# Kernel tuning notes

Hardware: AMD Instinct MI355X
Metric: run time of the kernel (lower is better)

Reference implementation:

```python
import jax, jax.numpy as jnp
import numpy as np

# Dims: B=4 batch, S=1024 seq, E=512 embed_dim, H=8 heads, K=3 gate lookback.
_B, _S, _E, _H, _K = 4, 1024, 512, 8, 3
_EPS_LN = 1e-5
_DIV_DELTA = 1e-12


def setup_inputs() -> dict:
    key = jax.random.key(0)
    ks = jax.random.split(key, 8)

    def w(k, shape, s=0.02):
        return jax.random.normal(k, shape, jnp.float32) * s

    return {
        "query": jax.random.normal(ks[0], (_B, _S, _E), jnp.float32),
        "ln1_g": jnp.ones((_E,), jnp.float32),
        "ln1_b": jnp.zeros((_E,), jnp.float32),
        "in_proj_w": w(ks[1], (3 * _E, _E)),          # packed W_q;W_k;W_v
        "in_proj_b": jnp.zeros((3 * _E,), jnp.float32),
        "out_w": w(ks[2], (_E, _H * _E)),             # out_proj: Linear(E*H -> E)
        "out_b": jnp.zeros((_E,), jnp.float32),
        "conv_w": w(ks[3], (_H, _E, _K)),             # SyntacticDistanceGate causal conv
        "conv_b": jnp.zeros((_H,), jnp.float32),
        "ln2_g": jnp.ones((_E,), jnp.float32),
        "ln2_b": jnp.zeros((_E,), jnp.float32),
        "mlp_w1": w(ks[4], (4 * _E, _E)),
        "mlp_b1": jnp.zeros((4 * _E,), jnp.float32),
        "mlp_w2": w(ks[5], (_E, 4 * _E)),
        "mlp_b2": jnp.zeros((_E,), jnp.float32),
    }


def _layer_norm(x, g, b):
    m = jnp.mean(x, axis=-1, keepdims=True)
    v = jnp.mean(jnp.square(x - m), axis=-1, keepdims=True)
    return (x - m) * jax.lax.rsqrt(v + _EPS_LN) * g + b


def _syntactic_gate(x, conv_w, conv_b):
    """x: [B,S,E] -> gate [B,H,S,S], distance [B,H,S].
    Causal depth-to-head conv produces per-head syntactic distances; gate is a
    smooth comparison sigmoid(d_i - d_j) (PRPN-style distance gating)."""
    K = conv_w.shape[-1]
    xp = jnp.pad(x, ((0, 0), (K - 1, 0), (0, 0)))  # causal left pad
    S = x.shape[1]
    d = conv_b[None, :, None]
    for k in range(K):  # tiny fixed lookback loop
        d = d + jnp.einsum("bse,he->bhs", xp[:, k:k + S, :], conv_w[:, :, k])
    distance = jnp.tanh(d)                               # [B,H,S]
    gate = jax.nn.sigmoid(distance[:, :, :, None] - distance[:, :, None, :])
    return gate, distance


def reference(query, ln1_g, ln1_b, in_proj_w, in_proj_b, out_w, out_b,
              conv_w, conv_b, ln2_g, ln2_b, mlp_w1, mlp_b1, mlp_w2, mlp_b2):
    B, S, E = query.shape
    H = conv_w.shape[0]

    nq = _layer_norm(query, ln1_g, ln1_b)  # self-attention: key=value=normed query

    gate, _distance = _syntactic_gate(nq, conv_w, conv_b)  # [B,H,S,S]

    # In-projections (heads are NOT split: each head sees full E-dim q/k/v).
    qkv = nq @ in_proj_w.T + in_proj_b          # [B,S,3E]
    q, k, v = jnp.split(qkv, 3, axis=-1)

    # Raw scores (scaled by sqrt(E), per source). Identical across heads since
    # q/k are merely repeated per head; compute once and broadcast over H.
    scores = jnp.einsum("bie,bje->bij", q, k) / jnp.sqrt(jnp.float32(E))

    # NOTE: with no key_padding_mask the source skips softmax entirely; the
    # gate multiplies RAW scores, then sum-normalizes.
    w = scores[:, None, :, :] * gate                       # [B,H,S,S]
    w = w / (jnp.sum(w, axis=-1, keepdims=True) + _DIV_DELTA)

    ctx = jnp.einsum("bhij,bje->bhie", w, v)               # [B,H,S,E]
    # torch: chunk over head-major dim 0 then cat on features -> [B,S,H*E]
    ctx = jnp.transpose(ctx, (0, 2, 1, 3)).reshape(B, S, H * E)
    attn_out = ctx @ out_w.T + out_b                       # [B,S,E]

    x = query + attn_out                                   # layer_scale_1 = Identity
    h = _layer_norm(x, ln2_g, ln2_b)
    h = jax.nn.gelu(h @ mlp_w1.T + mlp_b1, approximate=False)
    x = x + (h @ mlp_w2.T + mlp_b2)                        # layer_scale_2 = Identity
    return x
```

## Files before the change

### kernel.cpp

```cpp
#include <hip/hip_runtime.h>
#include <math.h>

#define SQ 1024
#define EE 512
#define NB 4
#define NH 8

typedef __attribute__((ext_vector_type(8))) short bfrag;
typedef __attribute__((ext_vector_type(4))) float f32x4;
typedef __attribute__((ext_vector_type(4))) unsigned short u16x4;
typedef __attribute__((ext_vector_type(8))) unsigned short u16x8;

typedef __attribute__((address_space(3))) unsigned int lds_u32;
typedef const __attribute__((address_space(1))) unsigned int glb_u32;

__device__ __forceinline__ float sep(float x) {
  asm volatile("" : "+v"(x));
  return x;
}

__device__ __forceinline__ unsigned short f2bf(float f) {
  unsigned u = __builtin_bit_cast(unsigned, f);
  unsigned r = (u + 0x7fffu + ((u >> 16) & 1u)) >> 16;
  return (unsigned short)r;
}
__device__ __forceinline__ float bf2f(unsigned short h) {
  unsigned u = ((unsigned)h) << 16;
  return __builtin_bit_cast(float, u);
}
__device__ __forceinline__ float bitf(unsigned u) { return __builtin_bit_cast(float, u); }

__device__ __forceinline__ unsigned cvtpk(float a, float b) {
  unsigned r;
  asm("v_cvt_pk_bf16_f32 %0, %1, %2" : "=v"(r) : "v"(a), "v"(b));
  return r;
}

__device__ __forceinline__ void split4(float4 v, u16x4& h, u16x4& l) {
  h.x = f2bf(v.x); l.x = f2bf(v.x - bf2f(h.x));
  h.y = f2bf(v.y); l.y = f2bf(v.y - bf2f(h.y));
  h.z = f2bf(v.z); l.z = f2bf(v.z - bf2f(h.z));
  h.w = f2bf(v.w); l.w = f2bf(v.w - bf2f(h.w));
}

__device__ __forceinline__ int swzi(int row, int c8) {
  return row * 40 + ((c8 ^ ((row >> 2) & 6)) << 2);
}

__global__ __launch_bounds__(64) void ln_np(const float* __restrict__ x,
                                            const float* __restrict__ g,
                                            const float* __restrict__ b,
                                            float* __restrict__ y) {
  __shared__ float xs[EE];
  __shared__ float bc[2];
  long long t = blockIdx.x;
  int lane = threadIdx.x;
#pragma unroll
  for (int m = 0; m < 8; m++) xs[lane + 64 * m] = x[t * EE + lane + 64 * m];
  __syncthreads();
  int l = lane >> 3, a = lane & 7;
  float r = 0.f;
  if (lane < 32) {
    r = xs[l * 128 + a];
#pragma unroll
    for (int m = 1; m < 16; m++) r = r + xs[l * 128 + 8 * m + a];
  }
  r = r + __shfl_xor(r, 1);
  r = r + __shfl_xor(r, 2);
  r = r + __shfl_xor(r, 4);
  r = r + __shfl_xor(r, 8);
  r = r + __shfl_xor(r, 16);
  if (lane == 0) bc[0] = r / 512.0f;
  __syncthreads();
  float mean = bc[0];
  r = 0.f;
  if (lane < 32) {
#pragma unroll
    for (int m = 0; m < 16; m++) {
      float d = sep(xs[l * 128 + 8 * m + a] - mean);
      float s2 = sep(d * d);
      r = (m == 0) ? s2 : (r + s2);
    }
  }
  r = r + __shfl_xor(r, 1);
  r = r + __shfl_xor(r, 2);
  r = r + __shfl_xor(r, 4);
  r = r + __shfl_xor(r, 8);
  r = r + __shfl_xor(r, 16);
  if (lane == 0) bc[1] = r / 512.0f;
  __syncthreads();
  float var = bc[1];
  float rs = 1.0f / sqrtf(var + 1e-5f);
#pragma unroll
  for (int m = 0; m < 8; m++) {
    int i = lane + 64 * m;
    float d = sep(xs[i] - mean);
    float t1 = sep(d * rs);
    float t2 = sep(t1 * g[i]);
    y[t * EE + i] = t2 + b[i];
  }
}

__global__ __launch_bounds__(64) void ln_np_s(const float* __restrict__ x,
                                              const float* __restrict__ g,
                                              const float* __restrict__ b,
                                              unsigned short* __restrict__ yh,
                                              unsigned short* __restrict__ yl) {
  __shared__ float xs[EE];
  __shared__ float bc[2];
  long long t = blockIdx.x;
  int lane = threadIdx.x;
#pragma unroll
  for (int m = 0; m < 8; m++) xs[lane + 64 * m] = x[t * EE + lane + 64 * m];
  __syncthreads();
  int l = lane >> 3, a = lane & 7;
  float r = 0.f;
  if (lane < 32) {
    r = xs[l * 128 + a];
#pragma unroll
    for (int m = 1; m < 16; m++) r = r + xs[l * 128 + 8 * m + a];
  }
  r = r + __shfl_xor(r, 1);
  r = r + __shfl_xor(r, 2);
  r = r + __shfl_xor(r, 4);
  r = r + __shfl_xor(r, 8);
  r = r + __shfl_xor(r, 16);
  if (lane == 0) bc[0] = r / 512.0f;
  __syncthreads();
  float mean = bc[0];
  r = 0.f;
  if (lane < 32) {
#pragma unroll
    for (int m = 0; m < 16; m++) {
      float d = sep(xs[l * 128 + 8 * m + a] - mean);
      float s2 = sep(d * d);
      r = (m == 0) ? s2 : (r + s2);
    }
  }
  r = r + __shfl_xor(r, 1);
  r = r + __shfl_xor(r, 2);
  r = r + __shfl_xor(r, 4);
  r = r + __shfl_xor(r, 8);
  r = r + __shfl_xor(r, 16);
  if (lane == 0) bc[1] = r / 512.0f;
  __syncthreads();
  float var = bc[1];
  float rs = 1.0f / sqrtf(var + 1e-5f);
#pragma unroll
  for (int m = 0; m < 8; m++) {
    int i = lane + 64 * m;
    float d = sep(xs[i] - mean);
    float t1 = sep(d * rs);
    float t2 = sep(t1 * g[i]);
    float o = t2 + b[i];
    unsigned short hh = f2bf(o);
    yh[t * EE + i] = hh;
    yl[t * EE + i] = f2bf(o - bf2f(hh));
  }
}

__global__ __launch_bounds__(256) void dist_np(const float* __restrict__ nq,
                                               const float* __restrict__ conv_w,
                                               const float* __restrict__ conv_b,
                                               float* __restrict__ dist,
                                               float* __restrict__ Edist) {
  int bh = blockIdx.x;
  int b = bh >> 3, h = bh & 7;
  float cb = conv_b[h];
  const float* W = conv_w + (long long)h * EE * 3;
  int s = blockIdx.y * 256 + threadIdx.x;
  float d = cb;
#pragma unroll
  for (int k = 0; k < 3; k++) {
    int t = s - 2 + k;
    if (t < 0) continue;
    const float* row = nq + ((long long)b * SQ + t) * EE;
    float acc = 0.f;
    for (int e = 0; e < EE; e++) acc = __builtin_fmaf(row[e], W[e * 3 + k], acc);
    d = sep(d + acc);
  }
  float dv = (float)tanh((double)d);
  dist[(long long)bh * SQ + s] = dv;
  Edist[(long long)bh * SQ + s] = __expf(dv);
}

__device__ __forceinline__ float gelu_exact(float x) {
  return 0.5f * x * (1.f + erff(x / 1.41421356237309504880f));
}

template <int ACT, int SPLITK>
__global__ __launch_bounds__(256) void gemm_nt(const float* __restrict__ A, int lda, long long sA,
                                               const float* __restrict__ B, int ldb, long long sB,
                                               const float* __restrict__ bias,
                                               const float* __restrict__ Res,
                                               float* __restrict__ C, int ldc, long long sC,
                                               int K, float alpha) {
  __shared__ float As[16][68];
  __shared__ float Bs[16][68];
  int z = blockIdx.z;
  A += (long long)z * sA;
  B += (long long)z * sB;
  C += (long long)z * sC;
  int m0 = blockIdx.y * 64, n0 = blockIdx.x * 64;
  int tid = threadIdx.x;
  int lr = tid >> 2, lc = tid & 3;
  int tx = tid & 15, ty = tid >> 4;
  float acc[4][4] = {};
  float acc2[4][4] = {};
  const float* Arow = A + (long long)(m0 + lr) * lda + lc * 4;
  const float* Brow = B + (long long)(n0 + lr) * ldb + lc * 4;
  float4 a4 = *(const float4*)(Arow);
  float4 b4 = *(const float4*)(Brow);
  for (int k0 = 0; k0 < K; k0 += 16) {
    __syncthreads();
    As[lc * 4 + 0][lr] = a4.x; As[lc * 4 + 1][lr] = a4.y;
    As[lc * 4 + 2][lr] = a4.z; As[lc * 4 + 3][lr] = a4.w;
    Bs[lc * 4 + 0][lr] = b4.x; Bs[lc * 4 + 1][lr] = b4.y;
    Bs[lc * 4 + 2][lr] = b4.z; Bs[lc * 4 + 3][lr] = b4.w;
    __syncthreads();
    int kn = (k0 + 16 < K) ? (k0 + 16) : k0;
    float4 a4n = *(const float4*)(Arow + kn);
    float4 b4n = *(const float4*)(Brow + kn);
    float(*tgt)[4] = (SPLITK > 0 && k0 >= SPLITK) ? acc2 : acc;
#pragma unroll
    for (int kk = 0; kk < 16; kk++) {
      float4 av = *(const float4*)&As[kk][ty * 4];
      float4 bv = *(const float4*)&Bs[kk][tx * 4];
      float a[4] = {av.x, av.y, av.z, av.w};
      float bb[4] = {bv.x, bv.y, bv.z, bv.w};
#pragma unroll
      for (int i = 0; i < 4; i++)
#pragma unroll
        for (int j = 0; j < 4; j++) tgt[i][j] += a[i] * bb[j];
    }
    a4 = a4n;
    b4 = b4n;
  }
  if (SPLITK > 0) {
#pragma unroll
    for (int i = 0; i < 4; i++)
#pragma unroll
      for (int j = 0; j < 4; j++) acc[i][j] = sep(acc[i][j]) + acc2[i][j];
  }
  float4 bias4 = make_float4(0.f, 0.f, 0.f, 0.f);
  if (ACT != 2 && bias) bias4 = *(const float4*)(bias + n0 + tx * 4);
#pragma unroll
  for (int i = 0; i < 4; i++) {
    int row = m0 + ty * 4 + i;
    float o[4];
    if (ACT == 2) {
#pragma unroll
      for (int j = 0; j < 4; j++) o[j] = acc[i][j] / alpha;
    } else {
      o[0] = sep(acc[i][0] * alpha) + bias4.x;
      o[1] = sep(acc[i][1] * alpha) + bias4.y;
      o[2] = sep(acc[i][2] * alpha) + bias4.z;
      o[3] = sep(acc[i][3] * alpha) + bias4.w;
    }
    if (ACT == 1) {
#pragma unroll
      for (int j = 0; j < 4; j++) o[j] = gelu_exact(o[j]);
    }
    if (Res) {
      float4 r4 = *(const float4*)(Res + (long long)row * ldc + n0 + tx * 4);
      o[0] = sep(o[0]) + r4.x; o[1] = sep(o[1]) + r4.y;
      o[2] = sep(o[2]) + r4.z; o[3] = sep(o[3]) + r4.w;
    }
    *(float4*)(C + (long long)row * ldc + n0 + tx * 4) = make_float4(o[0], o[1], o[2], o[3]);
  }
}

__global__ __launch_bounds__(64) void rowsum_np(const float* __restrict__ scores,
                                                const float* __restrict__ dist,
                                                float* __restrict__ invrs) {
  __shared__ float wsm[SQ];
  int i = blockIdx.x;
  int z = blockIdx.y;
  int b = z >> 3;
  const float* srow = scores + ((long long)b * SQ + i) * SQ;
  const float* dz = dist + (long long)z * SQ;
  float di = dz[i];
  int lane = threadIdx.x;
#pragma unroll
  for (int m = 0; m < 16; m++) {
    int j = lane + 64 * m;
    float e = (float)exp((double)(dz[j] - di));
    float gg = 1.f / (1.f + e);
    wsm[j] = srow[j] * gg;
  }
  __syncthreads();
  int l = lane >> 3, a = lane & 7;
  float r = wsm[l * 128 + a];
#pragma unroll
  for (int m = 1; m < 16; m++) r = r + wsm[l * 128 + 8 * m + a];
  r = r + __shfl_xor(r, 1);
  r = r + __shfl_xor(r, 2);
  r = r + __shfl_xor(r, 4);
  r = r + __shfl_xor(r, 8);
  r = r + __shfl_xor(r, 16);
  r = r + __shfl_xor(r, 32);
  if (lane == 0) invrs[(long long)z * SQ + i] = 1.f / (r + 1e-12f);
}

__global__ __launch_bounds__(256) void vsplit_t(const float* __restrict__ qkv,
                                                unsigned short* __restrict__ VhT,
                                                unsigned short* __restrict__ VlT) {
  __shared__ float tile[64][65];
  int b = blockIdx.z;
  int j0 = blockIdx.x * 64;
  int e0 = blockIdx.y * 64;
  const float* V = qkv + (long long)b * SQ * (3 * EE) + 2 * EE;
  unsigned short* Vh = VhT + (long long)b * EE * SQ;
  unsigned short* Vl = VlT + (long long)b * EE * SQ;
  int tx = threadIdx.x & 15, ty = threadIdx.x >> 4;
#pragma unroll
  for (int r = 0; r < 4; r++) {
    int j = j0 + ty + r * 16;
    float4 v = *(const float4*)(V + (long long)j * (3 * EE) + e0 + tx * 4);
    tile[ty + r * 16][tx * 4 + 0] = v.x;
    tile[ty + r * 16][tx * 4 + 1] = v.y;
    tile[ty + r * 16][tx * 4 + 2] = v.z;
    tile[ty + r * 16][tx * 4 + 3] = v.w;
  }
  __syncthreads();
#pragma unroll
  for (int r = 0; r < 4; r++) {
    int el = ty + r * 16;
    float4 f;
    f.x = tile[tx * 4 + 0][el];
    f.y = tile[tx * 4 + 1][el];
    f.z = tile[tx * 4 + 2][el];
    f.w = tile[tx * 4 + 3][el];
    u16x4 hh, ll;
    split4(f, hh, ll);
    long long o = (long long)(e0 + el) * SQ + j0 + tx * 4;
    *(u16x4*)(Vh + o) = hh;
    *(u16x4*)(Vl + o) = ll;
  }
}

__global__ __launch_bounds__(256) void wsplit(const float* __restrict__ W,
                                              unsigned short* __restrict__ Wh,
                                              unsigned short* __restrict__ Wl, int n4) {
  int i = blockIdx.x * 256 + threadIdx.x;
  if (i >= n4) return;
  float4 v = *(const float4*)(W + (long long)i * 4);
  u16x4 h, l;
  split4(v, h, l);
  *(u16x4*)(Wh + (long long)i * 4) = h;
  *(u16x4*)(Wl + (long long)i * 4) = l;
}

__global__ __launch_bounds__(256, 2) void ctx_bf3(const float* __restrict__ scores,
                                                  const float* __restrict__ Edist,
                                                  const float* __restrict__ invrs,
                                                  const unsigned short* __restrict__ VhT,
                                                  const unsigned short* __restrict__ VlT,
                                                  unsigned short* __restrict__ Ch,
                                                  unsigned short* __restrict__ Cl) {
  __shared__ __align__(16) unsigned short Ah[128 * 40], Al[128 * 40];
  __shared__ __align__(16) unsigned short Bh[256 * 40], Bl[256 * 40];
  int z = blockIdx.z, b = z >> 3, h = z & 7;
  const float* Sb = scores + (long long)b * SQ * SQ;
  const unsigned short* Vh = VhT + (long long)b * EE * SQ;
  const unsigned short* Vl = VlT + (long long)b * EE * SQ;
  unsigned short* Chb = Ch + (long long)b * SQ * (NH * EE) + h * EE;
  unsigned short* Clb = Cl + (long long)b * SQ * (NH * EE) + h * EE;
  const float* Ez = Edist + (long long)z * SQ;
  int m0 = blockIdx.y * 128, n0 = blockIdx.x * 256;
  int tid = threadIdx.x;
  int wave = tid >> 6, lane = tid & 63;
  int quad = lane >> 4, l16 = lane & 15;
  f32x4 acc[4][8];
#pragma unroll
  for (int mf = 0; mf < 4; mf++)
#pragma unroll
    for (int nf = 0; nf < 8; nf++) acc[mf][nf] = (f32x4)(0.f);

  int aam = tid & 127, aakc = tid >> 7;
  float ei = Ez[m0 + aam];
  float inv = invrs[(long long)z * SQ + m0 + aam];
  float ci = ei * inv;
  const float* Srow = Sb + (long long)(m0 + aam) * SQ;
  int brow = tid;
  const unsigned short* VhRow = Vh + (long long)(n0 + brow) * SQ;
  const unsigned short* VlRow = Vl + (long long)(n0 + brow) * SQ;

  uint2 aHp[4], aLp[4];
  u16x8 bH[4], bL[4];

  auto loadconv = [&](int kb) {
#pragma unroll
    for (int r = 0; r < 4; r++) {
      int kc = aakc * 4 + r;
      float4 s4 = *(const float4*)(Srow + kb + kc * 4);
      float4 e4 = *(const float4*)(Ez + kb + kc * 4);
      float ax = (s4.x * ci) * __builtin_amdgcn_rcpf(ei + e4.x);
      float ay = (s4.y * ci) * __builtin_amdgcn_rcpf(ei + e4.y);
      float az = (s4.z * ci) * __builtin_amdgcn_rcpf(ei + e4.z);
      float aw = (s4.w * ci) * __builtin_amdgcn_rcpf(ei + e4.w);
      unsigned h01 = cvtpk(ax, ay), h23 = cvtpk(az, aw);
      float hx = bitf(h01 << 16), hy = bitf(h01 & 0xffff0000u);
      float hz = bitf(h23 << 16), hw = bitf(h23 & 0xffff0000u);
      unsigned l01 = cvtpk(ax - hx, ay - hy), l23 = cvtpk(az - hz, aw - hw);
      aHp[r] = make_uint2(h01, h23);
      aLp[r] = make_uint2(l01, l23);
    }
#pragma unroll
    for (int c = 0; c < 4; c++) {
      bH[c] = *(const u16x8*)(VhRow + kb + c * 8);
      bL[c] = *(const u16x8*)(VlRow + kb + c * 8);
    }
  };

  loadconv(0);
  for (int k0 = 0; k0 < SQ; k0 += 32) {
    __syncthreads();
#pragma unroll
    for (int r = 0; r < 4; r++) {
      *(uint2*)&Ah[swzi(aam, aakc * 4 + r)] = aHp[r];
      *(uint2*)&Al[swzi(aam, aakc * 4 + r)] = aLp[r];
    }
#pragma unroll
    for (int c = 0; c < 4; c++) {
      *(u16x8*)&Bh[swzi(brow, 2 * c)] = bH[c];
      *(u16x8*)&Bl[swzi(brow, 2 * c)] = bL[c];
    }
    __syncthreads();
    int kn = (k0 + 32 < SQ) ? (k0 + 32) : k0;
    loadconv(kn);
    bfrag ah[4], al_[4];
#pragma unroll
    for (int mf = 0; mf < 4; mf++) {
      int ra = (wave >> 1) * 64 + mf * 16 + l16;
      ah[mf] = *(const bfrag*)&Ah[swzi(ra, quad * 2)];
      al_[mf] = *(const bfrag*)&Al[swzi(ra, quad * 2)];
    }
#pragma unroll
    for (int nf = 0; nf < 8; nf++) {
      int rb = (wave & 1) * 128 + nf * 16 + l16;
      bfrag bh = *(const bfrag*)&Bh[swzi(rb, quad * 2)];
      bfrag bl = *(const bfrag*)&Bl[swzi(rb, quad * 2)];
#pragma unroll
      for (int mf = 0; mf < 4; mf++) {
        acc[mf][nf] = __builtin_amdgcn_mfma_f32_16x16x32_bf16(al_[mf], bh, acc[mf][nf], 0, 0, 0);
        acc[mf][nf] = __builtin_amdgcn_mfma_f32_16x16x32_bf16(ah[mf], bl, acc[mf][nf], 0, 0, 0);
        acc[mf][nf] = __builtin_amdgcn_mfma_f32_16x16x32_bf16(ah[mf], bh, acc[mf][nf], 0, 0, 0);
      }
    }
  }
#pragma unroll
  for (int mf = 0; mf < 4; mf++) {
#pragma unroll
    for (int nf = 0; nf < 8; nf++) {
      int col = n0 + (wave & 1) * 128 + nf * 16 + l16;
#pragma unroll
      for (int r = 0; r < 4; r++) {
        int row = m0 + (wave >> 1) * 64 + mf * 16 + quad * 4 + r;
        float o = acc[mf][nf][r];
        unsigned short hh = f2bf(o);
        Chb[(long long)row * (NH * EE) + col] = hh;
        Clb[(long long)row * (NH * EE) + col] = f2bf(o - bf2f(hh));
      }
    }
  }
}

template <int ACT, int OUTM>
__global__ __launch_bounds__(256) void gemm_bf3w(
    const unsigned short* __restrict__ Ah_g, const unsigned short* __restrict__ Al_g, int lda,
    const unsigned short* __restrict__ Bh_g, const unsigned short* __restrict__ Bl_g, int ldb,
    const float* __restrict__ bias, const float* __restrict__ Res,
    float* __restrict__ C, unsigned short* __restrict__ Ch, unsigned short* __restrict__ Cl,
    int ldc, int K) {
  __shared__ __align__(16) unsigned short lds[3 * 12288];
  int gx = gridDim.x;
  int nwg = gx * (int)gridDim.y;
  int lin = blockIdx.y * gx + blockIdx.x;
  int cpx = nwg >> 3;
  int tl = (lin & 7) * cpx + (lin >> 3);
  int bx = tl % gx, by = tl / gx;
  int m0 = by * 128, n0 = bx * 64;
  int tid = threadIdx.x, wave = tid >> 6, lane = tid & 63;
  int quad = lane >> 4, l16 = lane & 15;

  const unsigned short* gptr[6];
  int ldsoff[6];
#pragma unroll
  for (int i = 0; i < 6; i++) {
    int d = wave * 6 + i;
    const unsigned short* src;
    int rowbase, ld, tb, qt;
    if (d < 8)       { src = Ah_g; rowbase = m0; ld = lda; tb = 0;     qt = d; }
    else if (d < 16) { src = Al_g; rowbase = m0; ld = lda; tb = 4096;  qt = d - 8; }
    else if (d < 20) { src = Bh_g; rowbase = n0; ld = ldb; tb = 8192;  qt = d - 16; }
    else             { src = Bl_g; rowbase = n0; ld = ldb; tb = 10240; qt = d - 20; }
    int row = qt * 16 + (lane >> 2);
    int cG = (lane & 3) ^ ((row >> 1) & 3);
    gptr[i] = src + (long long)(rowbase + row) * ld + cG * 8;
    ldsoff[i] = tb + qt * 512;
  }

  auto stage = [&](int buf, int kb) {
#pragma unroll
    for (int i = 0; i < 6; i++)
      __builtin_amdgcn_global_load_lds((glb_u32*)(gptr[i] + kb),
                                       (lds_u32*)&lds[buf * 12288 + ldsoff[i]], 16, 0, 0);
  };

  int aoff[4], boff[2];
#pragma unroll
  for (int mf = 0; mf < 4; mf++) {
    int r = (wave >> 1) * 64 + mf * 16 + l16;
    aoff[mf] = r * 32 + ((quad ^ ((r >> 1) & 3)) * 8);
  }
#pragma unroll
  for (int nf = 0; nf < 2; nf++) {
    int r = (wave & 1) * 32 + nf * 16 + l16;
    boff[nf] = r * 32 + ((quad ^ ((r >> 1) & 3)) * 8);
  }

  f32x4 acc[4][2];
#pragma unroll
  for (int mf = 0; mf < 4; mf++)
#pragma unroll
    for (int nf = 0; nf < 2; nf++) acc[mf][nf] = (f32x4)(0.f);

  int NT = K >> 5;
  stage(0, 0);
  stage(1, 32);
  int cur = 0;
  for (int t = 0; t < NT; t++) {
    int nb = cur + 2; if (nb >= 3) nb -= 3;
    int kf = (t + 2 < NT) ? (t + 2) * 32 : (NT - 1) * 32;
    stage(nb, kf);
    asm volatile("s_waitcnt vmcnt(12)" ::: "memory");
    __builtin_amdgcn_s_barrier();
    __builtin_amdgcn_sched_barrier(0);
    const unsigned short* L = &lds[cur * 12288];
    bfrag bh[2], bl[2];
#pragma unroll
    for (int nf = 0; nf < 2; nf++) {
      bh[nf] = *(const bfrag*)&L[8192 + boff[nf]];
      bl[nf] = *(const bfrag*)&L[10240 + boff[nf]];
    }
#pragma unroll
    for (int mf = 0; mf < 4; mf++) {
      bfrag ah = *(const bfrag*)&L[aoff[mf]];
      bfrag al = *(const bfrag*)&L[4096 + aoff[mf]];
#pragma unroll
      for (int nf = 0; nf < 2; nf++) {
        acc[mf][nf] = __builtin_amdgcn_mfma_f32_16x16x32_bf16(al, bh[nf], acc[mf][nf], 0, 0, 0);
        acc[mf][nf] = __builtin_amdgcn_mfma_f32_16x16x32_bf16(ah, bl[nf], acc[mf][nf], 0, 0, 0);
        acc[mf][nf] = __builtin_amdgcn_mfma_f32_16x16x32_bf16(ah, bh[nf], acc[mf][nf], 0, 0, 0);
      }
    }
    __builtin_amdgcn_sched_barrier(0);
    __builtin_amdgcn_s_barrier();
    cur++; if (cur >= 3) cur -= 3;
  }

#pragma unroll
  for (int mf = 0; mf < 4; mf++) {
#pragma unroll
    for (int nf = 0; nf < 2; nf++) {
      int col = n0 + (wave & 1) * 32 + nf * 16 + l16;
      float bi = bias ? bias[col] : 0.f;
#pragma unroll
      for (int r = 0; r < 4; r++) {
        int row = m0 + (wave >> 1) * 64 + mf * 16 + quad * 4 + r;
        float o = acc[mf][nf][r] + bi;
        if (ACT == 1) o = gelu_exact(o);
        if (OUTM == 0) {
          if (Res) o = o + Res[(long long)row * ldc + col];
          C[(long long)row * ldc + col] = o;
        } else {
          unsigned short hh = f2bf(o);
          Ch[(long long)row * ldc + col] = hh;
          Cl[(long long)row * ldc + col] = f2bf(o - bf2f(hh));
        }
      }
    }
  }
}

extern "C" void kernel_launch(void* const* d_in, const int* in_sizes, int n_in,
                              void* d_out, int out_size, void* d_ws, size_t ws_size,
                              hipStream_t stream) {
  const float* query     = (const float*)d_in[0];
  const float* ln1_g     = (const float*)d_in[1];
  const float* ln1_b     = (const float*)d_in[2];
  const float* in_proj_w = (const float*)d_in[3];
  const float* in_proj_b = (const float*)d_in[4];
  const float* out_w     = (const float*)d_in[5];
  const float* out_b     = (const float*)d_in[6];
  const float* conv_w    = (const float*)d_in[7];
  const float* conv_b    = (const float*)d_in[8];
  const float* ln2_g     = (const float*)d_in[9];
  const float* ln2_b     = (const float*)d_in[10];
  const float* mlp_w1    = (const float*)d_in[11];
  const float* mlp_b1    = (const float*)d_in[12];
  const float* mlp_w2    = (const float*)d_in[13];
  const float* mlp_b2    = (const float*)d_in[14];
  float* out = (float*)d_out;
  char* ws = (char*)d_ws;

  float* nq     = (float*)(ws + 0);
  float* qkv    = (float*)(ws + (8ull << 20));
  float* dist   = (float*)(ws + (32ull << 20));
  float* invrs  = (float*)(ws + (32ull << 20) + 131072);
  float* scores = (float*)(ws + (32ull << 20) + 262144);
  unsigned short* VhT = (unsigned short*)(ws + 0);
  unsigned short* VlT = (unsigned short*)(ws + (4ull << 20));
  unsigned short* ctxh = (unsigned short*)(ws + (48ull << 20) + 262144);
  unsigned short* ctxl = (unsigned short*)(ws + (80ull << 20) + 262144);
  unsigned short* out_wh = (unsigned short*)(ws + (32ull << 20) + 262144);
  unsigned short* out_wl = out_wh + 2097152;
  unsigned short* w1h    = out_wl + 2097152;
  unsigned short* w1l    = w1h + 1048576;
  unsigned short* w2h    = w1l + 1048576;
  unsigned short* w2l    = w2h + 1048576;
  unsigned short* ln2h = (unsigned short*)(ws + (48ull << 20) + 262144);
  unsigned short* ln2l = ln2h + 2097152;
  unsigned short* hbufh = (unsigned short*)(ws + 0);
  unsigned short* hbufl = hbufh + 8388608;
  float* Edist = (float*)d_out;

  ln_np<<<dim3(NB * SQ), 64, 0, stream>>>(query, ln1_g, ln1_b, nq);
  dist_np<<<dim3(NB * NH, 4), 256, 0, stream>>>(nq, conv_w, conv_b, dist, Edist);
  gemm_nt<0, 384><<<dim3(24, 64, 1), 256, 0, stream>>>(nq, EE, 0, in_proj_w, EE, 0,
                                                       in_proj_b, nullptr, qkv, 3 * EE, 0, EE, 1.f);
  vsplit_t<<<dim3(16, 8, NB), 256, 0, stream>>>(qkv, VhT, VlT);
  gemm_nt<2, 384><<<dim3(16, 16, NB), 256, 0, stream>>>(
      qkv, 3 * EE, (long long)SQ * 3 * EE, qkv + EE, 3 * EE, (long long)SQ * 3 * EE,
      nullptr, nullptr, scores, SQ, (long long)SQ * SQ, EE, sqrtf(512.0f));
  rowsum_np<<<dim3(SQ, NB * NH), 64, 0, stream>>>(scores, dist, invrs);
  ctx_bf3<<<dim3(2, 8, NB * NH), 256, 0, stream>>>(scores, Edist, invrs, VhT, VlT, ctxh, ctxl);
  wsplit<<<dim3(2048), 256, 0, stream>>>(out_w, out_wh, out_wl, 524288);
  wsplit<<<dim3(1024), 256, 0, stream>>>(mlp_w1, w1h, w1l, 262144);
  wsplit<<<dim3(1024), 256, 0, stream>>>(mlp_w2, w2h, w2l, 262144);
  gemm_bf3w<0, 0><<<dim3(8, 32), 256, 0, stream>>>(ctxh, ctxl, NH * EE, out_wh, out_wl, NH * EE,
                                                   out_b, query, out, nullptr, nullptr,
                                                   EE, NH * EE);
  ln_np_s<<<dim3(NB * SQ), 64, 0, stream>>>(out, ln2_g, ln2_b, ln2h, ln2l);
  gemm_bf3w<1, 1><<<dim3(32, 32), 256, 0, stream>>>(ln2h, ln2l, EE, w1h, w1l, EE,
                                                    mlp_b1, nullptr, nullptr, hbufh, hbufl,
                                                    4 * EE, EE);
  gemm_bf3w<0, 0><<<dim3(8, 32), 256, 0, stream>>>(hbufh, hbufl, 4 * EE, w2h, w2l, 4 * EE,
                                                   mlp_b2, out, out, nullptr, nullptr,
                                                   EE, 4 * EE);
}
```

Before: 669.4 us.

## Split-K two-group GEMM for long-K projections and 512-thread ctx kernel

Adds gemm_bf3w2, which runs two 256-thread groups per block, each covering half of K with its own triple-buffered LDS pipeline. The two partial sums are reduced through LDS before the epilogue. It is used for the out_proj and MLP-down GEMMs, which have a long K and only 256 blocks each. Separately, ctx_bf3 moves to 512 threads with 8 waves on a 2x4 wave grid, smaller per-wave tiles, an unpadded XOR-swizzled LDS layout and precomputed offsets. The goal is more waves in flight to hide latency, at the cost of doubled LDS use per block and an extra reduction step.

```diff
diff --git a/kernel.cpp b/kernel.cpp
--- a/kernel.cpp
+++ b/kernel.cpp
@@ -41,10 +41,6 @@
   h.y = f2bf(v.y); l.y = f2bf(v.y - bf2f(h.y));
   h.z = f2bf(v.z); l.z = f2bf(v.z - bf2f(h.z));
   h.w = f2bf(v.w); l.w = f2bf(v.w - bf2f(h.w));
-}
-
-__device__ __forceinline__ int swzi(int row, int c8) {
-  return row * 40 + ((c8 ^ ((row >> 2) & 6)) << 2);
 }
 
 __global__ __launch_bounds__(64) void ln_np(const float* __restrict__ x,
@@ -351,15 +347,15 @@
   *(u16x4*)(Wl + (long long)i * 4) = l;
 }
 
-__global__ __launch_bounds__(256, 2) void ctx_bf3(const float* __restrict__ scores,
-                                                  const float* __restrict__ Edist,
-                                                  const float* __restrict__ invrs,
-                                                  const unsigned short* __restrict__ VhT,
-                                                  const unsigned short* __restrict__ VlT,
-                                                  unsigned short* __restrict__ Ch,
-                                                  unsigned short* __restrict__ Cl) {
-  __shared__ __align__(16) unsigned short Ah[128 * 40], Al[128 * 40];
-  __shared__ __align__(16) unsigned short Bh[256 * 40], Bl[256 * 40];
+__global__ __launch_bounds__(512) void ctx_bf3(const float* __restrict__ scores,
+                                               const float* __restrict__ Edist,
+                                               const float* __restrict__ invrs,
+                                               const unsigned short* __restrict__ VhT,
+                                               const unsigned short* __restrict__ VlT,
+                                               unsigned short* __restrict__ Ch,
+                                               unsigned short* __restrict__ Cl) {
+  __shared__ __align__(16) unsigned short Ah[128 * 32], Al[128 * 32];
+  __shared__ __align__(16) unsigned short Bh[256 * 32], Bl[256 * 32];
   int z = blockIdx.z, b = z >> 3, h = z & 7;
   const float* Sb = scores + (long long)b * SQ * SQ;
   const unsigned short* Vh = VhT + (long long)b * EE * SQ;
@@ -371,28 +367,29 @@
   int tid = threadIdx.x;
   int wave = tid >> 6, lane = tid & 63;
   int quad = lane >> 4, l16 = lane & 15;
-  f32x4 acc[4][8];
+  int wr = wave >> 2, wc = wave & 3;
+  f32x4 acc[4][4];
 #pragma unroll
   for (int mf = 0; mf < 4; mf++)
 #pragma unroll
-    for (int nf = 0; nf < 8; nf++) acc[mf][nf] = (f32x4)(0.f);
+    for (int nf = 0; nf < 4; nf++) acc[mf][nf] = (f32x4)(0.f);
 
   int aam = tid & 127, aakc = tid >> 7;
   float ei = Ez[m0 + aam];
   float inv = invrs[(long long)z * SQ + m0 + aam];
   float ci = ei * inv;
   const float* Srow = Sb + (long long)(m0 + aam) * SQ;
-  int brow = tid;
+  int brow = tid & 255, bk8 = tid >> 8;
   const unsigned short* VhRow = Vh + (long long)(n0 + brow) * SQ;
   const unsigned short* VlRow = Vl + (long long)(n0 + brow) * SQ;
 
-  uint2 aHp[4], aLp[4];
-  u16x8 bH[4], bL[4];
+  uint2 aHp[2], aLp[2];
+  u16x8 bH[2], bL[2];
 
   auto loadconv = [&](int kb) {
 #pragma unroll
-    for (int r = 0; r < 4; r++) {
-      int kc = aakc * 4 + r;
+    for (int r = 0; r < 2; r++) {
+      int kc = aakc * 2 + r;
       float4 s4 = *(const float4*)(Srow + kb + kc * 4);
       float4 e4 = *(const float4*)(Ez + kb + kc * 4);
       float ax = (s4.x * ci) * __builtin_amdgcn_rcpf(ei + e4.x);
@@ -407,24 +404,44 @@
       aLp[r] = make_uint2(l01, l23);
     }
 #pragma unroll
-    for (int c = 0; c < 4; c++) {
-      bH[c] = *(const u16x8*)(VhRow + kb + c * 8);
-      bL[c] = *(const u16x8*)(VlRow + kb + c * 8);
+    for (int r = 0; r < 2; r++) {
+      bH[r] = *(const u16x8*)(VhRow + kb + (bk8 * 2 + r) * 8);
+      bL[r] = *(const u16x8*)(VlRow + kb + (bk8 * 2 + r) * 8);
     }
   };
+
+  int offA = aam * 32 + ((aakc ^ ((aam >> 1) & 3)) * 8);
+  int offB[2];
+#pragma unroll
+  for (int r = 0; r < 2; r++) {
+    int c = bk8 * 2 + r;
+    offB[r] = brow * 32 + ((c ^ ((brow >> 1) & 3)) * 8);
+  }
+  int aoff[4], boff[4];
+#pragma unroll
+  for (int mf = 0; mf < 4; mf++) {
+    int ra = wr * 64 + mf * 16 + l16;
+    aoff[mf] = ra * 32 + ((quad ^ ((ra >> 1) & 3)) * 8);
+  }
+#pragma unroll
+  for (int nf = 0; nf < 4; nf++) {
+    int rb = wc * 64 + nf * 16 + l16;
+    boff[nf] = rb * 32 + ((quad ^ ((rb >> 1) & 3)) * 8);
+  }
 
   loadconv(0);
   for (int k0 = 0; k0 < SQ; k0 += 32) {
     __syncthreads();
-#pragma unroll
-    for (int r = 0; r < 4; r++) {
-      *(uint2*)&Ah[swzi(aam, aakc * 4 + r)] = aHp[r];
-      *(uint2*)&Al[swzi(aam, aakc * 4 + r)] = aLp[r];
-    }
-#pragma unroll
-    for (int c = 0; c < 4; c++) {
-      *(u16x8*)&Bh[swzi(brow, 2 * c)] = bH[c];
-      *(u16x8*)&Bl[swzi(brow, 2 * c)] = bL[c];
+    {
+      uint4 hv = make_uint4(aHp[0].x, aHp[0].y, aHp[1].x, aHp[1].y);
+      uint4 lv = make_uint4(aLp[0].x, aLp[0].y, aLp[1].x, aLp[1].y);
+      *(uint4*)&Ah[offA] = hv;
+      *(uint4*)&Al[offA] = lv;
+    }
+#pragma unroll
+    for (int r = 0; r < 2; r++) {
+      *(u16x8*)&Bh[offB[r]] = bH[r];
+      *(u16x8*)&Bl[offB[r]] = bL[r];
     }
     __syncthreads();
     int kn = (k0 + 32 < SQ) ? (k0 + 32) : k0;
@@ -432,15 +449,13 @@
     bfrag ah[4], al_[4];
 #pragma unroll
     for (int mf = 0; mf < 4; mf++) {
-      int ra = (wave >> 1) * 64 + mf * 16 + l16;
-      ah[mf] = *(const bfrag*)&Ah[swzi(ra, quad * 2)];
-      al_[mf] = *(const bfrag*)&Al[swzi(ra, quad * 2)];
-    }
-#pragma unroll
-    for (int nf = 0; nf < 8; nf++) {
-      int rb = (wave & 1) * 128 + nf * 16 + l16;
-      bfrag bh = *(const bfrag*)&Bh[swzi(rb, quad * 2)];
-      bfrag bl = *(const bfrag*)&Bl[swzi(rb, quad * 2)];
+      ah[mf] = *(const bfrag*)&Ah[aoff[mf]];
+      al_[mf] = *(const bfrag*)&Al[aoff[mf]];
+    }
+#pragma unroll
+    for (int nf = 0; nf < 4; nf++) {
+      bfrag bh = *(const bfrag*)&Bh[boff[nf]];
+      bfrag bl = *(const bfrag*)&Bl[boff[nf]];
 #pragma unroll
       for (int mf = 0; mf < 4; mf++) {
         acc[mf][nf] = __builtin_amdgcn_mfma_f32_16x16x32_bf16(al_[mf], bh, acc[mf][nf], 0, 0, 0);
@@ -452,11 +467,11 @@
 #pragma unroll
   for (int mf = 0; mf < 4; mf++) {
 #pragma unroll
-    for (int nf = 0; nf < 8; nf++) {
-      int col = n0 + (wave & 1) * 128 + nf * 16 + l16;
+    for (int nf = 0; nf < 4; nf++) {
+      int col = n0 + wc * 64 + nf * 16 + l16;
 #pragma unroll
       for (int r = 0; r < 4; r++) {
-        int row = m0 + (wave >> 1) * 64 + mf * 16 + quad * 4 + r;
+        int row = m0 + wr * 64 + mf * 16 + quad * 4 + r;
         float o = acc[mf][nf][r];
         unsigned short hh = f2bf(o);
         Chb[(long long)row * (NH * EE) + col] = hh;
@@ -578,6 +593,149 @@
           unsigned short hh = f2bf(o);
           Ch[(long long)row * ldc + col] = hh;
           Cl[(long long)row * ldc + col] = f2bf(o - bf2f(hh));
+        }
+      }
+    }
+  }
+}
+
+template <int ACT, int OUTM>
+__global__ __launch_bounds__(512) void gemm_bf3w2(
+    const unsigned short* __restrict__ Ah_g, const unsigned short* __restrict__ Al_g, int lda,
+    const unsigned short* __restrict__ Bh_g, const unsigned short* __restrict__ Bl_g, int ldb,
+    const float* __restrict__ bias, const float* __restrict__ Res,
+    float* __restrict__ C, unsigned short* __restrict__ Ch, unsigned short* __restrict__ Cl,
+    int ldc, int K) {
+  __shared__ __align__(16) unsigned short lds[2][3 * 12288];
+  int gx = gridDim.x;
+  int nwg = gx * (int)gridDim.y;
+  int lin = blockIdx.y * gx + blockIdx.x;
+  int cpx = nwg >> 3;
+  int tl = (lin & 7) * cpx + (lin >> 3);
+  int bx = tl % gx, by = tl / gx;
+  int m0 = by * 128, n0 = bx * 64;
+  int tid = threadIdx.x;
+  int grp = tid >> 8, gtid = tid & 255;
+  int wave = gtid >> 6, lane = tid & 63;
+  int quad = lane >> 4, l16 = lane & 15;
+  int kbase = grp * (K >> 1);
+
+  const unsigned short* gptr[6];
+  int ldsoff[6];
+#pragma unroll
+  for (int i = 0; i < 6; i++) {
+    int d = wave * 6 + i;
+    const unsigned short* src;
+    int rowbase, ld, tb, qt;
+    if (d < 8)       { src = Ah_g; rowbase = m0; ld = lda; tb = 0;     qt = d; }
+    else if (d < 16) { src = Al_g; rowbase = m0; ld = lda; tb = 4096;  qt = d - 8; }
+    else if (d < 20) { src = Bh_g; rowbase = n0; ld = ldb; tb = 8192;  qt = d - 16; }
+    else             { src = Bl_g; rowbase = n0; ld = ldb; tb = 10240; qt = d - 20; }
+    int row = qt * 16 + (lane >> 2);
+    int cG = (lane & 3) ^ ((row >> 1) & 3);
+    gptr[i] = src + (long long)(rowbase + row) * ld + cG * 8;
+    ldsoff[i] = tb + qt * 512;
+  }
+
+  auto stage = [&](int buf, int kb) {
+#pragma unroll
+    for (int i = 0; i < 6; i++)
+      __builtin_amdgcn_global_load_lds((glb_u32*)(gptr[i] + kb),
+                                       (lds_u32*)&lds[grp][buf * 12288 + ldsoff[i]], 16, 0, 0);
+  };
+
+  int aoff[4], boff[2];
+#pragma unroll
+  for (int mf = 0; mf < 4; mf++) {
+    int r = (wave >> 1) * 64 + mf * 16 + l16;
+    aoff[mf] = r * 32 + ((quad ^ ((r >> 1) & 3)) * 8);
+  }
+#pragma unroll
+  for (int nf = 0; nf < 2; nf++) {
+    int r = (wave & 1) * 32 + nf * 16 + l16;
+    boff[nf] = r * 32 + ((quad ^ ((r >> 1) & 3)) * 8);
+  }
+
+  f32x4 acc[4][2];
+#pragma unroll
+  for (int mf = 0; mf < 4; mf++)
+#pragma unroll
+    for (int nf = 0; nf < 2; nf++) acc[mf][nf] = (f32x4)(0.f);
+
+  int NT = (K >> 1) >> 5;
+  stage(0, kbase);
+  stage(1, kbase + 32);
+  int cur = 0;
+  for (int t = 0; t < NT; t++) {
+    int nb = cur + 2; if (nb >= 3) nb -= 3;
+    int kf = (t + 2 < NT) ? (t + 2) * 32 : (NT - 1) * 32;
+    stage(nb, kbase + kf);
+    asm volatile("s_waitcnt vmcnt(12)" ::: "memory");
+    __builtin_amdgcn_s_barrier();
+    __builtin_amdgcn_sched_barrier(0);
+    const unsigned short* L = &lds[grp][cur * 12288];
+    bfrag bh[2], bl[2];
+#pragma unroll
+    for (int nf = 0; nf < 2; nf++) {
+      bh[nf] = *(const bfrag*)&L[8192 + boff[nf]];
+      bl[nf] = *(const bfrag*)&L[10240 + boff[nf]];
+    }
+#pragma unroll
+    for (int mf = 0; mf < 4; mf++) {
+      bfrag ah = *(const bfrag*)&L[aoff[mf]];
+      bfrag al = *(const bfrag*)&L[4096 + aoff[mf]];
+#pragma unroll
+      for (int nf = 0; nf < 2; nf++) {
+        acc[mf][nf] = __builtin_amdgcn_mfma_f32_16x16x32_bf16(al, bh[nf], acc[mf][nf], 0, 0, 0);
+        acc[mf][nf] = __builtin_amdgcn_mfma_f32_16x16x32_bf16(ah, bl[nf], acc[mf][nf], 0, 0, 0);
+        acc[mf][nf] = __builtin_amdgcn_mfma_f32_16x16x32_bf16(ah, bh[nf], acc[mf][nf], 0, 0, 0);
+      }
+    }
+    __builtin_amdgcn_sched_barrier(0);
+    __builtin_amdgcn_s_barrier();
+    cur++; if (cur >= 3) cur -= 3;
+  }
+
+  asm volatile("s_waitcnt vmcnt(0)" ::: "memory");
+  __syncthreads();
+  float* red = (float*)&lds[1][0];
+  if (grp == 1) {
+#pragma unroll
+    for (int mf = 0; mf < 4; mf++)
+#pragma unroll
+      for (int nf = 0; nf < 2; nf++)
+#pragma unroll
+        for (int r = 0; r < 4; r++)
+          red[(((mf * 2 + nf) * 4) + r) * 256 + gtid] = acc[mf][nf][r];
+  }
+  __syncthreads();
+  if (grp == 0) {
+#pragma unroll
+    for (int mf = 0; mf < 4; mf++)
+#pragma unroll
+      for (int nf = 0; nf < 2; nf++)
+#pragma unroll
+        for (int r = 0; r < 4; r++)
+          acc[mf][nf][r] += red[(((mf * 2 + nf) * 4) + r) * 256 + gtid];
+#pragma unroll
+    for (int mf = 0; mf < 4; mf++) {
+#pragma unroll
+      for (int nf = 0; nf < 2; nf++) {
+        int col = n0 + (wave & 1) * 32 + nf * 16 + l16;
+        float bi = bias ? bias[col] : 0.f;
+#pragma unroll
+        for (int r = 0; r < 4; r++) {
+          int row = m0 + (wave >> 1) * 64 + mf * 16 + quad * 4 + r;
+          float o = acc[mf][nf][r] + bi;
+          if (ACT == 1) o = gelu_exact(o);
+          if (OUTM == 0) {
+            if (Res) o = o + Res[(long long)row * ldc + col];
+            C[(long long)row * ldc + col] = o;
+          } else {
+            unsigned short hh = f2bf(o);
+            Ch[(long long)row * ldc + col] = hh;
+            Cl[(long long)row * ldc + col] = f2bf(o - bf2f(hh));
+          }
         }
       }
     }
@@ -635,18 +793,18 @@
       qkv, 3 * EE, (long long)SQ * 3 * EE, qkv + EE, 3 * EE, (long long)SQ * 3 * EE,
       nullptr, nullptr, scores, SQ, (long long)SQ * SQ, EE, sqrtf(512.0f));
   rowsum_np<<<dim3(SQ, NB * NH), 64, 0, stream>>>(scores, dist, invrs);
-  ctx_bf3<<<dim3(2, 8, NB * NH), 256, 0, stream>>>(scores, Edist, invrs, VhT, VlT, ctxh, ctxl);
+  ctx_bf3<<<dim3(2, 8, NB * NH), 512, 0, stream>>>(scores, Edist, invrs, VhT, VlT, ctxh, ctxl);
   wsplit<<<dim3(2048), 256, 0, stream>>>(out_w, out_wh, out_wl, 524288);
   wsplit<<<dim3(1024), 256, 0, stream>>>(mlp_w1, w1h, w1l, 262144);
   wsplit<<<dim3(1024), 256, 0, stream>>>(mlp_w2, w2h, w2l, 262144);
-  gemm_bf3w<0, 0><<<dim3(8, 32), 256, 0, stream>>>(ctxh, ctxl, NH * EE, out_wh, out_wl, NH * EE,
-                                                   out_b, query, out, nullptr, nullptr,
-                                                   EE, NH * EE);
+  gemm_bf3w2<0, 0><<<dim3(8, 32), 512, 0, stream>>>(ctxh, ctxl, NH * EE, out_wh, out_wl, NH * EE,
+                                                    out_b, query, out, nullptr, nullptr,
+                                                    EE, NH * EE);
   ln_np_s<<<dim3(NB * SQ), 64, 0, stream>>>(out, ln2_g, ln2_b, ln2h, ln2l);
   gemm_bf3w<1, 1><<<dim3(32, 32), 256, 0, stream>>>(ln2h, ln2l, EE, w1h, w1l, EE,
                                                     mlp_b1, nullptr, nullptr, hbufh, hbufl,
                                                     4 * EE, EE);
-  gemm_bf3w<0, 0><<<dim3(8, 32), 256, 0, stream>>>(hbufh, hbufl, 4 * EE, w2h, w2l, 4 * EE,
-                                                   mlp_b2, out, out, nullptr, nullptr,
-                                                   EE, 4 * EE);
-}
+  gemm_bf3w2<0, 0><<<dim3(8, 32), 512, 0, stream>>>(hbufh, hbufl, 4 * EE, w2h, w2l, 4 * EE,
+                                                    mlp_b2, out, out, nullptr, nullptr,
+                                                    EE, 4 * EE);
+}
```

After: 696.5 us. 1.04x slower.

## Double-buffer V tiles via direct global-to-LDS loads in ctx kernel

Applied to the files above, without the earlier changes.

The ctx_bf3 kernel now stages the V hi/lo tiles straight from global memory into a double-buffered LDS region using global_load_lds, instead of going through registers. The LDS layout changes from a padded row stride to an unpadded stride with an XOR swizzle. Gate computation for the A operand is split from its global loads and moved after the barrier so it overlaps the MFMA work. Manual waitcnt and sched_barrier calls control the ordering. This aims to cut register pressure and VMEM-to-LDS staging cost, but it doubles B-tile LDS use and depends on hand-tuned wait counts being correct.

```diff
diff --git a/kernel.cpp b/kernel.cpp
--- a/kernel.cpp
+++ b/kernel.cpp
@@ -41,10 +41,6 @@
   h.y = f2bf(v.y); l.y = f2bf(v.y - bf2f(h.y));
   h.z = f2bf(v.z); l.z = f2bf(v.z - bf2f(h.z));
   h.w = f2bf(v.w); l.w = f2bf(v.w - bf2f(h.w));
-}
-
-__device__ __forceinline__ int swzi(int row, int c8) {
-  return row * 40 + ((c8 ^ ((row >> 2) & 6)) << 2);
 }
 
 __global__ __launch_bounds__(64) void ln_np(const float* __restrict__ x,
@@ -358,8 +354,8 @@
                                                   const unsigned short* __restrict__ VlT,
                                                   unsigned short* __restrict__ Ch,
                                                   unsigned short* __restrict__ Cl) {
-  __shared__ __align__(16) unsigned short Ah[128 * 40], Al[128 * 40];
-  __shared__ __align__(16) unsigned short Bh[256 * 40], Bl[256 * 40];
+  __shared__ __align__(16) unsigned short Ah[128 * 32], Al[128 * 32];
+  __shared__ __align__(16) unsigned short Bh[2][256 * 32], Bl[2][256 * 32];
   int z = blockIdx.z, b = z >> 3, h = z & 7;
   const float* Sb = scores + (long long)b * SQ * SQ;
   const unsigned short* Vh = VhT + (long long)b * EE * SQ;
@@ -371,6 +367,7 @@
   int tid = threadIdx.x;
   int wave = tid >> 6, lane = tid & 63;
   int quad = lane >> 4, l16 = lane & 15;
+  int wr = wave >> 1, wc = wave & 1;
   f32x4 acc[4][8];
 #pragma unroll
   for (int mf = 0; mf < 4; mf++)
@@ -382,19 +379,51 @@
   float inv = invrs[(long long)z * SQ + m0 + aam];
   float ci = ei * inv;
   const float* Srow = Sb + (long long)(m0 + aam) * SQ;
-  int brow = tid;
-  const unsigned short* VhRow = Vh + (long long)(n0 + brow) * SQ;
-  const unsigned short* VlRow = Vl + (long long)(n0 + brow) * SQ;
-
-  uint2 aHp[4], aLp[4];
-  u16x8 bH[4], bL[4];
-
-  auto loadconv = [&](int kb) {
+  int offA[2];
+#pragma unroll
+  for (int cc = 0; cc < 2; cc++) {
+    int c = aakc * 2 + cc;
+    offA[cc] = aam * 32 + ((c ^ ((aam >> 1) & 3)) * 8);
+  }
+
+  const unsigned short* gB = (wave < 2) ? Vh : Vl;
+  long long gbase[8];
+  int ldsq[8];
+#pragma unroll
+  for (int i = 0; i < 8; i++) {
+    int qt = (wave & 1) * 8 + i;
+    int row = qt * 16 + (lane >> 2);
+    int cG = (lane & 3) ^ ((row >> 1) & 3);
+    gbase[i] = (long long)(n0 + row) * SQ + cG * 8;
+    ldsq[i] = qt * 512;
+  }
+
+  int aoff[4], boff[8];
+#pragma unroll
+  for (int mf = 0; mf < 4; mf++) {
+    int ra = wr * 64 + mf * 16 + l16;
+    aoff[mf] = ra * 32 + ((quad ^ ((ra >> 1) & 3)) * 8);
+  }
+#pragma unroll
+  for (int nf = 0; nf < 8; nf++) {
+    int rb = wc * 128 + nf * 16 + l16;
+    boff[nf] = rb * 32 + ((quad ^ ((rb >> 1) & 3)) * 8);
+  }
+
+  float4 s4r[4], e4r[4];
+  uint4 aHc[2], aLc[2];
+  auto loadA = [&](int kb) {
 #pragma unroll
     for (int r = 0; r < 4; r++) {
       int kc = aakc * 4 + r;
-      float4 s4 = *(const float4*)(Srow + kb + kc * 4);
-      float4 e4 = *(const float4*)(Ez + kb + kc * 4);
+      s4r[r] = *(const float4*)(Srow + kb + kc * 4);
+      e4r[r] = *(const float4*)(Ez + kb + kc * 4);
+    }
+  };
+  auto gateA = [&]() {
+#pragma unroll
+    for (int r = 0; r < 4; r++) {
+      float4 s4 = s4r[r], e4 = e4r[r];
       float ax = (s4.x * ci) * __builtin_amdgcn_rcpf(ei + e4.x);
       float ay = (s4.y * ci) * __builtin_amdgcn_rcpf(ei + e4.y);
       float az = (s4.z * ci) * __builtin_amdgcn_rcpf(ei + e4.z);
@@ -403,44 +432,53 @@
       float hx = bitf(h01 << 16), hy = bitf(h01 & 0xffff0000u);
       float hz = bitf(h23 << 16), hw = bitf(h23 & 0xffff0000u);
       unsigned l01 = cvtpk(ax - hx, ay - hy), l23 = cvtpk(az - hz, aw - hw);
-      aHp[r] = make_uint2(h01, h23);
-      aLp[r] = make_uint2(l01, l23);
-    }
-#pragma unroll
-    for (int c = 0; c < 4; c++) {
-      bH[c] = *(const u16x8*)(VhRow + kb + c * 8);
-      bL[c] = *(const u16x8*)(VlRow + kb + c * 8);
+      if ((r & 1) == 0) {
+        aHc[r >> 1].x = h01; aHc[r >> 1].y = h23;
+        aLc[r >> 1].x = l01; aLc[r >> 1].y = l23;
+      } else {
+        aHc[r >> 1].z = h01; aHc[r >> 1].w = h23;
+        aLc[r >> 1].z = l01; aLc[r >> 1].w = l23;
+      }
     }
   };
-
-  loadconv(0);
-  for (int k0 = 0; k0 < SQ; k0 += 32) {
-    __syncthreads();
-#pragma unroll
-    for (int r = 0; r < 4; r++) {
-      *(uint2*)&Ah[swzi(aam, aakc * 4 + r)] = aHp[r];
-      *(uint2*)&Al[swzi(aam, aakc * 4 + r)] = aLp[r];
-    }
-#pragma unroll
-    for (int c = 0; c < 4; c++) {
-      *(u16x8*)&Bh[swzi(brow, 2 * c)] = bH[c];
-      *(u16x8*)&Bl[swzi(brow, 2 * c)] = bL[c];
-    }
-    __syncthreads();
-    int kn = (k0 + 32 < SQ) ? (k0 + 32) : k0;
-    loadconv(kn);
+  auto stageB = [&](int buf, int kb) {
+    unsigned short* base = (wave < 2) ? &Bh[buf][0] : &Bl[buf][0];
+#pragma unroll
+    for (int i = 0; i < 8; i++)
+      __builtin_amdgcn_global_load_lds((glb_u32*)(gB + gbase[i] + kb),
+                                       (lds_u32*)(base + ldsq[i]), 16, 0, 0);
+  };
+
+  loadA(0);
+  gateA();
+  stageB(0, 0);
+  constexpr int NT = SQ / 32;
+  for (int t = 0; t < NT; t++) {
+    int cur = t & 1;
+    __builtin_amdgcn_s_barrier();
+#pragma unroll
+    for (int cc = 0; cc < 2; cc++) {
+      *(uint4*)&Ah[offA[cc]] = aHc[cc];
+      *(uint4*)&Al[offA[cc]] = aLc[cc];
+    }
+    int kn = (t + 1 < NT) ? (t + 1) * 32 : t * 32;
+    loadA(kn);
+    stageB(cur ^ 1, kn);
+    asm volatile("s_waitcnt lgkmcnt(0)" ::: "memory");
+    asm volatile("s_waitcnt vmcnt(16)" ::: "memory");
+    __builtin_amdgcn_s_barrier();
+    __builtin_amdgcn_sched_barrier(0);
+    gateA();
     bfrag ah[4], al_[4];
 #pragma unroll
     for (int mf = 0; mf < 4; mf++) {
-      int ra = (wave >> 1) * 64 + mf * 16 + l16;
-      ah[mf] = *(const bfrag*)&Ah[swzi(ra, quad * 2)];
-      al_[mf] = *(const bfrag*)&Al[swzi(ra, quad * 2)];
+      ah[mf] = *(const bfrag*)&Ah[aoff[mf]];
+      al_[mf] = *(const bfrag*)&Al[aoff[mf]];
     }
 #pragma unroll
     for (int nf = 0; nf < 8; nf++) {
-      int rb = (wave & 1) * 128 + nf * 16 + l16;
-      bfrag bh = *(const bfrag*)&Bh[swzi(rb, quad * 2)];
-      bfrag bl = *(const bfrag*)&Bl[swzi(rb, quad * 2)];
+      bfrag bh = *(const bfrag*)&Bh[cur][boff[nf]];
+      bfrag bl = *(const bfrag*)&Bl[cur][boff[nf]];
 #pragma unroll
       for (int mf = 0; mf < 4; mf++) {
         acc[mf][nf] = __builtin_amdgcn_mfma_f32_16x16x32_bf16(al_[mf], bh, acc[mf][nf], 0, 0, 0);
@@ -448,15 +486,16 @@
         acc[mf][nf] = __builtin_amdgcn_mfma_f32_16x16x32_bf16(ah[mf], bh, acc[mf][nf], 0, 0, 0);
       }
     }
+    __builtin_amdgcn_sched_barrier(0);
   }
 #pragma unroll
   for (int mf = 0; mf < 4; mf++) {
 #pragma unroll
     for (int nf = 0; nf < 8; nf++) {
-      int col = n0 + (wave & 1) * 128 + nf * 16 + l16;
+      int col = n0 + wc * 128 + nf * 16 + l16;
 #pragma unroll
       for (int r = 0; r < 4; r++) {
-        int row = m0 + (wave >> 1) * 64 + mf * 16 + quad * 4 + r;
+        int row = m0 + wr * 64 + mf * 16 + quad * 4 + r;
         float o = acc[mf][nf][r];
         unsigned short hh = f2bf(o);
         Chb[(long long)row * (NH * EE) + col] = hh;
```

After: 657.3 us. About the same (-1.8%).
